# Kernel tuning notes

Measured on AMD Instinct MI355X. Metric: run time of the kernel, lower is better.

## Reference

```python
import jax, jax.numpy as jnp
import numpy as np

DIM = 1024
DIM_HEAD = 64
HEADS = 8
INNER = DIM_HEAD * HEADS
EPS = 1e-5


def layernorm(x, g, b):
    mu = jnp.mean(x, axis=-1, keepdims=True)
    var = jnp.var(x, axis=-1, keepdims=True)
    return (x - mu) * jax.lax.rsqrt(var + EPS) * g + b


def setup_inputs() -> dict:
    key = jax.random.key(0)
    ks = jax.random.split(key, 8)
    b, n, m = 8, 4096, 64
    x = jax.random.normal(ks[0], (b, n, DIM), dtype=jnp.float32)
    latents = jax.random.normal(ks[1], (b, m, DIM), dtype=jnp.float32)
    mask = jax.random.bernoulli(ks[2], 0.9, (b, n))
    s = DIM ** -0.5
    Wq = jax.random.normal(ks[3], (DIM, INNER), dtype=jnp.float32) * s
    Wkv = jax.random.normal(ks[4], (DIM, 2 * INNER), dtype=jnp.float32) * s
    Wo = jax.random.normal(ks[5], (INNER, DIM), dtype=jnp.float32) * (INNER ** -0.5)
    ln_x_g = jnp.ones((DIM,), jnp.float32); ln_x_b = jnp.zeros((DIM,), jnp.float32)
    ln_l_g = jnp.ones((DIM,), jnp.float32); ln_l_b = jnp.zeros((DIM,), jnp.float32)
    ln_o_g = jnp.ones((DIM,), jnp.float32); ln_o_b = jnp.zeros((DIM,), jnp.float32)
    return {"x": x, "latents": latents, "mask": mask,
            "Wq": Wq, "Wkv": Wkv, "Wo": Wo,
            "ln_x_g": ln_x_g, "ln_x_b": ln_x_b,
            "ln_l_g": ln_l_g, "ln_l_b": ln_l_b,
            "ln_o_g": ln_o_g, "ln_o_b": ln_o_b}


def reference(x, latents, mask, Wq, Wkv, Wo, ln_x_g, ln_x_b, ln_l_g, ln_l_b, ln_o_g, ln_o_b):
    scale = DIM_HEAD ** -0.5
    b, m = latents.shape[0], latents.shape[1]
    xn = layernorm(x, ln_x_g, ln_x_b)
    ln = layernorm(latents, ln_l_g, ln_l_b)
    q = ln @ Wq                                   # [b, m, inner]
    kv_in = jnp.concatenate([xn, ln], axis=1)     # [b, n+m, dim]
    kv = kv_in @ Wkv                              # [b, n+m, 2*inner]
    k, v = jnp.split(kv, 2, axis=-1)
    # b n (h d) -> b h n d
    q = q.reshape(b, m, HEADS, DIM_HEAD).transpose(0, 2, 1, 3)
    k = k.reshape(b, k.shape[1], HEADS, DIM_HEAD).transpose(0, 2, 1, 3)
    v = v.reshape(b, v.shape[1], HEADS, DIM_HEAD).transpose(0, 2, 1, 3)
    # NOTE: scale applied twice, faithful to the original module.
    sim = jnp.einsum('bhid,bhjd->bhij', q * scale, k) * scale
    full_mask = jnp.concatenate([mask, jnp.ones((b, m), dtype=bool)], axis=1)  # pad True for latents
    max_neg = -jnp.finfo(sim.dtype).max
    sim = jnp.where(full_mask[:, None, None, :], sim, max_neg)
    attn = jax.nn.softmax(sim.astype(jnp.float32), axis=-1).astype(sim.dtype)
    out = jnp.einsum('bhij,bhjd->bhid', attn, v)
    out = out.transpose(0, 2, 1, 3).reshape(b, m, INNER)
    out = out @ Wo
    return layernorm(out, ln_o_g, ln_o_b)
```

## Files before the change

### kernel.cpp

```cpp
#include <hip/hip_runtime.h>

typedef unsigned short u16;
typedef unsigned int u32;
using f32x4  = __attribute__((ext_vector_type(4))) float;
using short8 = __attribute__((ext_vector_type(8))) short;
using s16x4  = __attribute__((ext_vector_type(4))) short;
using u16x4  = __attribute__((ext_vector_type(4))) unsigned short;

#define DEV __device__ __forceinline__

DEV u16 f2bf(float f) {
  u32 u = __float_as_uint(f);
  u32 r = u + 0x7fffu + ((u >> 16) & 1u);
  return (u16)(r >> 16);
}

DEV void gload_lds16(const void* g, void* l) {
  __builtin_amdgcn_global_load_lds(
      (__attribute__((address_space(1))) void*)g,
      (__attribute__((address_space(3))) void*)l, 16, 0, 0);
}

DEV void block_reduce2(float& a, float& b, float* red) {
#pragma unroll
  for (int m = 1; m < 64; m <<= 1) {
    a += __shfl_xor(a, m);
    b += __shfl_xor(b, m);
  }
  const int wid = threadIdx.x >> 6, lane = threadIdx.x & 63;
  __syncthreads();
  if (lane == 0) { red[wid] = a; red[4 + wid] = b; }
  __syncthreads();
  a = red[0] + red[1] + red[2] + red[3];
  b = red[4] + red[5] + red[6] + red[7];
}

__global__ __launch_bounds__(256) void ln_rows_k(
    const float* __restrict__ X, const float* __restrict__ g,
    const float* __restrict__ be, u16* __restrict__ out, int mode)
{
  __shared__ float red[8];
  const int r = blockIdx.x, t = threadIdx.x;
  const float4 v = *(const float4*)(X + (((size_t)r) << 10) + t * 4);
  float s1 = v.x + v.y + v.z + v.w;
  float s2 = v.x * v.x + v.y * v.y + v.z * v.z + v.w * v.w;
  block_reduce2(s1, s2, red);
  const float mean = s1 * (1.f / 1024.f);
  const float var  = s2 * (1.f / 1024.f) - mean * mean;
  const float rstd = rsqrtf(var + 1e-5f);
  const float4 gv = *(const float4*)(g + t * 4);
  const float4 bv = *(const float4*)(be + t * 4);
  u16x4 o;
  o[0] = f2bf((v.x - mean) * rstd * gv.x + bv.x);
  o[1] = f2bf((v.y - mean) * rstd * gv.y + bv.y);
  o[2] = f2bf((v.z - mean) * rstd * gv.z + bv.z);
  o[3] = f2bf((v.w - mean) * rstd * gv.w + bv.w);
  const size_t orow = (mode == 0)
      ? ((size_t)(r >> 12) * 4160 + (r & 4095))
      : ((size_t)(r >> 6) * 4160 + 4096 + (r & 63));
  *(u16x4*)(out + orow * 1024 + t * 4) = o;
}

__global__ __launch_bounds__(256) void transpose_w_k(
    const float* __restrict__ W, u16* __restrict__ Wt, int K, int N)
{
  __shared__ float tile[32][33];
  const int n0 = blockIdx.x * 32, k0 = blockIdx.y * 32;
  const int tx = threadIdx.x, ty = threadIdx.y;
#pragma unroll
  for (int i = 0; i < 4; ++i)
    tile[ty + 8 * i][tx] = W[(size_t)(k0 + ty + 8 * i) * N + n0 + tx];
  __syncthreads();
#pragma unroll
  for (int i = 0; i < 4; ++i)
    Wt[(size_t)(n0 + ty + 8 * i) * K + k0 + tx] = f2bf(tile[tx][ty + 8 * i]);
}

__global__ __launch_bounds__(256) void mask_bias_k(const void* __restrict__ mask,
                                                   float* __restrict__ bias)
{
  __shared__ int flag_s;
  if (threadIdx.x == 0) {
    const u32* mw = (const u32*)mask;
    bool fpat = true, ipat = true;
    for (int i = 0; i < 256; ++i) {
      u32 w = mw[i];
      if (w != 0u && w != 0x3f800000u) fpat = false;
      if (w > 1u) ipat = false;
    }
    flag_s = fpat ? 2 : (ipat ? 1 : 0);
  }
  __syncthreads();
  const int flag = flag_s;
  const int idx = blockIdx.x * 256 + threadIdx.x;
  const int b = idx / 4160, j = idx - b * 4160;
  float bv = 0.f;
  if (j < 4096) {
    const int mi = b * 4096 + j;
    bool on;
    if (flag == 2)      on = ((const float*)mask)[mi] != 0.f;
    else if (flag == 1) on = ((const int*)mask)[mi] != 0;
    else                on = ((const unsigned char*)mask)[mi] != 0;
    bv = on ? 0.f : -1e30f;
  }
  bias[idx] = bv;
}

__global__ __launch_bounds__(512, 4) void gemm2_k(
    const u16* __restrict__ xnl, const u16* __restrict__ Wq_t,
    const u16* __restrict__ Wkv_t,
    u16* __restrict__ q_h, u16* __restrict__ k_h, u16* __restrict__ v_t)
{
  __shared__ __attribute__((aligned(16))) short As[3][4096];
  __shared__ __attribute__((aligned(16))) short Bs[3][8192];

  const int tid = threadIdx.x, lane = tid & 63;
  const int wid = tid >> 6, wr = wid >> 2, wc = wid & 3;
  const int l15 = lane & 15, lq = lane >> 4;

  const int bid = blockIdx.x;
  int mode, mblk, nblk;
  const u16 *Ap, *Bp;
  if (bid < 1040) {
    const int slab = bid >> 3, s = bid & 7;
    if (s < 4) { mode = 0; mblk = slab * 2 + (s & 1); nblk = s >> 1; Ap = xnl; Bp = Wkv_t; }
    else       { mode = 2; mblk = s - 4; nblk = slab; Ap = Wkv_t + (size_t)512 * 1024; Bp = xnl; }
  } else {
    const int r2 = bid - 1040; mode = 1; mblk = r2 >> 1; nblk = r2 & 1;
    Ap = xnl; Bp = Wq_t;
  }
  const int m0 = mblk * 128, n0 = nblk * 256;

  const int srow = tid >> 2, sslot = tid & 3;
  const u32 ss = (u32)((sslot ^ ((srow >> 1) & 3)) * 8);
  const int gra = m0 + srow;
  const u32 arow = (mode == 1) ? ((u32)(gra >> 6) * 4160u + 4096u + (u32)(gra & 63)) : (u32)gra;
  const u32 aoff  = arow * 1024u + ss;
  const u32 boff0 = (u32)(n0 + srow) * 1024u + ss;
  const u32 boff1 = (u32)(n0 + 128 + srow) * 1024u + ss;

  const int rsw = ((lq ^ ((l15 >> 1) & 3)) << 4);
  const int aRd = wr * 4096 + l15 * 64 + rsw;
  const int bRd = wc * 4096 + l15 * 64 + rsw;

  const f32x4 z4 = {0.f, 0.f, 0.f, 0.f};
  f32x4 acc[4][4];
#pragma unroll
  for (int i = 0; i < 4; ++i)
#pragma unroll
    for (int j = 0; j < 4; ++j) acc[i][j] = z4;

  auto stage = [&](int buf, int T) {
    gload_lds16(Ap + aoff  + (u32)T * 32u, &As[buf][tid * 8]);
    gload_lds16(Bp + boff0 + (u32)T * 32u, &Bs[buf][tid * 8]);
    gload_lds16(Bp + boff1 + (u32)T * 32u, &Bs[buf][4096 + tid * 8]);
  };

  stage(0, 0);
  stage(1, 1);
  asm volatile("s_waitcnt vmcnt(3)" ::: "memory");
  __builtin_amdgcn_s_barrier();

  int c0 = 0, c1 = 1, c2 = 2;
#pragma unroll 1
  for (int t = 0; t < 32; ++t) {
    if (t < 30) stage(c2, t + 2);
    const char* aB = (const char*)&As[0][0] + c0 * 8192  + aRd;
    const char* bB = (const char*)&Bs[0][0] + c0 * 16384 + bRd;
    short8 af[4], bf[4];
#pragma unroll
    for (int mi = 0; mi < 4; ++mi) af[mi] = *(const short8*)(aB + mi * 1024);
#pragma unroll
    for (int nj = 0; nj < 4; ++nj) bf[nj] = *(const short8*)(bB + nj * 1024);
    __builtin_amdgcn_s_setprio(1);
#pragma unroll
    for (int mi = 0; mi < 4; ++mi)
#pragma unroll
      for (int nj = 0; nj < 4; ++nj)
        acc[mi][nj] = __builtin_amdgcn_mfma_f32_16x16x32_bf16(af[mi], bf[nj], acc[mi][nj], 0, 0, 0);
    __builtin_amdgcn_s_setprio(0);
    if (t < 30)       { asm volatile("s_waitcnt vmcnt(3)" ::: "memory"); }
    else if (t == 30) { asm volatile("s_waitcnt vmcnt(0)" ::: "memory"); }
    __builtin_amdgcn_s_barrier();
    const int tmp = c0; c0 = c1; c1 = c2; c2 = tmp;
  }

#pragma unroll
  for (int mi = 0; mi < 4; ++mi)
#pragma unroll
    for (int nj = 0; nj < 4; ++nj)
#pragma unroll
      for (int r = 0; r < 4; ++r) {
        const int gm = m0 + wr * 64 + mi * 16 + lq * 4 + r;
        const int gn = n0 + wc * 64 + nj * 16 + l15;
        const u16 v = f2bf(acc[mi][nj][r]);
        if (mode == 0) {
          const int b = gm / 4160, j = gm - b * 4160;
          k_h[(((size_t)b * 8 + (gn >> 6)) * 4160 + j) * 64 + (gn & 63)] = v;
        } else if (mode == 2) {
          const int b = gn / 4160, j = gn - b * 4160;
          v_t[(((size_t)b * 8 + (gm >> 6)) * 64 + (gm & 63)) * 4160 + j] = v;
        } else {
          const int b = gm >> 6, i2 = gm & 63;
          q_h[(((size_t)b * 8 + (gn >> 6)) * 64 + i2) * 64 + (gn & 63)] = v;
        }
      }
}

__global__ __launch_bounds__(256) void attn_k(
    const u16* __restrict__ q_h, const u16* __restrict__ k_h,
    const u16* __restrict__ v_t, const float* __restrict__ bias,
    float* __restrict__ O_part, float* __restrict__ m_part,
    float* __restrict__ l_part)
{
  __shared__ __attribute__((aligned(16))) short Ks[4096];
  __shared__ __attribute__((aligned(16))) short Vs[4096];
  __shared__ __attribute__((aligned(16))) short Ps[4][1152];
  __shared__ float biasS[64];
  const int bid = blockIdx.x;
  const int sp = bid & 7, bh = bid >> 3;
  const int b = bh >> 3;
  const int tid = threadIdx.x, wid = tid >> 6, lane = tid & 63;
  const int t0 = sp ? (8 * sp + 1) : 0;
  const int tc = sp ? 8 : 9;

  const size_t qoff = ((size_t)bh * 64 + wid * 16 + (lane & 15)) * 64 + 8 * (lane >> 4);
  const short8 qf0 = *(const short8*)&q_h[qoff];
  const short8 qf1 = *(const short8*)&q_h[qoff + 32];

  float mrun = -1e30f, lrun = 0.f;
  const f32x4 z4 = {0.f, 0.f, 0.f, 0.f};
  f32x4 o[4] = {z4, z4, z4, z4};
  const size_t khead = (size_t)bh * (4160 * 64);
  const size_t vhead = (size_t)bh * (64 * 4160);

  for (int tt = 0; tt < tc; ++tt) {
    const int t = t0 + tt;
#pragma unroll
    for (int p = 0; p < 2; ++p) {
      const int lo = (p * 256 + tid) * 16;
      const int row = lo >> 7;
      const int src = lo ^ ((row & 7) << 4);
      gload_lds16((const char*)k_h + (khead + (size_t)t * 4096) * 2 + src,
                  (char*)Ks + (p * 256 + wid * 64) * 16);
    }
#pragma unroll
    for (int p = 0; p < 2; ++p) {
      const int lo = (p * 256 + tid) * 16;
      const int row = lo >> 7;
      const int colb = (lo ^ ((row & 7) << 4)) & 127;
      gload_lds16((const char*)v_t + (vhead + (size_t)row * 4160 + t * 64) * 2 + colb,
                  (char*)Vs + (p * 256 + wid * 64) * 16);
    }
    if (tid < 64) biasS[tid] = bias[b * 4160 + t * 64 + tid];
    __syncthreads();

    f32x4 sc[4] = {z4, z4, z4, z4};
#pragma unroll
    for (int mi = 0; mi < 4; ++mi) {
      const int row = mi * 16 + (lane & 15);
      const int sw = (row & 7) << 4;
      short8 a0 = *(const short8*)((const char*)Ks + ((row * 128 + 16 * (lane >> 4)) ^ sw));
      sc[mi] = __builtin_amdgcn_mfma_f32_16x16x32_bf16(a0, qf0, sc[mi], 0, 0, 0);
      short8 a1 = *(const short8*)((const char*)Ks + ((row * 128 + 64 + 16 * (lane >> 4)) ^ sw));
      sc[mi] = __builtin_amdgcn_mfma_f32_16x16x32_bf16(a1, qf1, sc[mi], 0, 0, 0);
    }

    float sv[4][4];
    float tmax = -3e30f;
#pragma unroll
    for (int mi = 0; mi < 4; ++mi)
#pragma unroll
      for (int r = 0; r < 4; ++r) {
        const int kv = mi * 16 + (lane >> 4) * 4 + r;
        const float s = sc[mi][r] * (1.f / 64.f) + biasS[kv];
        sv[mi][r] = s;
        tmax = fmaxf(tmax, s);
      }
    tmax = fmaxf(tmax, __shfl_xor(tmax, 16));
    tmax = fmaxf(tmax, __shfl_xor(tmax, 32));
    const float mnew = fmaxf(mrun, tmax);
    const float fac = __expf(mrun - mnew);
    float psum = 0.f;
#pragma unroll
    for (int mi = 0; mi < 4; ++mi) {
      s16x4 pk;
#pragma unroll
      for (int r = 0; r < 4; ++r) {
        const float p = __expf(sv[mi][r] - mnew);
        psum += p;
        pk[r] = (short)f2bf(p);
      }
      *(s16x4*)&Ps[wid][(lane & 15) * 72 + mi * 16 + (lane >> 4) * 4] = pk;
    }
    psum += __shfl_xor(psum, 16);
    psum += __shfl_xor(psum, 32);
    lrun = lrun * fac + psum;
    mrun = mnew;
#pragma unroll
    for (int mi = 0; mi < 4; ++mi)
#pragma unroll
      for (int e = 0; e < 4; ++e) o[mi][e] *= fac;

#pragma unroll
    for (int mi = 0; mi < 4; ++mi) {
      const int row = mi * 16 + (lane & 15);
      const int sw = (row & 7) << 4;
      short8 a0 = *(const short8*)((const char*)Vs + ((row * 128 + 16 * (lane >> 4)) ^ sw));
      short8 p0 = *(const short8*)&Ps[wid][(lane & 15) * 72 + 8 * (lane >> 4)];
      o[mi] = __builtin_amdgcn_mfma_f32_16x16x32_bf16(a0, p0, o[mi], 0, 0, 0);
      short8 a1 = *(const short8*)((const char*)Vs + ((row * 128 + 64 + 16 * (lane >> 4)) ^ sw));
      short8 p1 = *(const short8*)&Ps[wid][(lane & 15) * 72 + 32 + 8 * (lane >> 4)];
      o[mi] = __builtin_amdgcn_mfma_f32_16x16x32_bf16(a1, p1, o[mi], 0, 0, 0);
    }
    __syncthreads();
  }

#pragma unroll
  for (int mi = 0; mi < 4; ++mi)
#pragma unroll
    for (int r = 0; r < 4; ++r) {
      const int d = mi * 16 + (lane >> 4) * 4 + r;
      const int q = wid * 16 + (lane & 15);
      O_part[(((size_t)sp * 64 + bh) * 64 + d) * 64 + q] = o[mi][r];
    }
  if (lane < 16) {
    m_part[((size_t)sp * 64 + bh) * 64 + wid * 16 + lane] = mrun;
    l_part[((size_t)sp * 64 + bh) * 64 + wid * 16 + lane] = lrun;
  }
}

__global__ __launch_bounds__(256) void combine_k(
    const float* __restrict__ O_part, const float* __restrict__ m_part,
    const float* __restrict__ l_part, float* __restrict__ attn_out)
{
  __shared__ float wgt[8][64];
  const int bh = blockIdx.x;
  const int b = bh >> 3, h = bh & 7;
  const int t = threadIdx.x;
  if (t < 64) {
    float mv[8], lv[8];
#pragma unroll
    for (int s = 0; s < 8; ++s) {
      mv[s] = m_part[((size_t)s * 64 + bh) * 64 + t];
      lv[s] = l_part[((size_t)s * 64 + bh) * 64 + t];
    }
    float M = mv[0];
#pragma unroll
    for (int s = 1; s < 8; ++s) M = fmaxf(M, mv[s]);
    float den = 0.f;
#pragma unroll
    for (int s = 0; s < 8; ++s) den += lv[s] * __expf(mv[s] - M);
    const float inv = 1.f / den;
#pragma unroll
    for (int s = 0; s < 8; ++s) wgt[s][t] = __expf(mv[s] - M) * inv;
  }
  __syncthreads();
#pragma unroll
  for (int i = 0; i < 16; ++i) {
    const int p = i * 256 + t;
    const int d = p >> 6, q = p & 63;
    float acc = 0.f;
#pragma unroll
    for (int s = 0; s < 8; ++s)
      acc += O_part[(((size_t)s * 64 + bh) * 64 + d) * 64 + q] * wgt[s][q];
    attn_out[((size_t)b * 64 + q) * 512 + h * 64 + d] = acc;
  }
}

__global__ __launch_bounds__(256) void outproj_k(
    const float* __restrict__ attn_out, const float* __restrict__ Wo,
    const float* __restrict__ g, const float* __restrict__ be,
    float* __restrict__ out)
{
  __shared__ float arow[2][512];
  __shared__ float red[8];
  const int rb = blockIdx.x * 2, t = threadIdx.x;
  arow[0][t]       = attn_out[(size_t)rb * 512 + t];
  arow[0][t + 256] = attn_out[(size_t)rb * 512 + 256 + t];
  arow[1][t]       = attn_out[(size_t)(rb + 1) * 512 + t];
  arow[1][t + 256] = attn_out[(size_t)(rb + 1) * 512 + 256 + t];
  __syncthreads();
  float a0x = 0, a0y = 0, a0z = 0, a0w = 0;
  float a1x = 0, a1y = 0, a1z = 0, a1w = 0;
  for (int k = 0; k < 512; ++k) {
    const float4 w = *(const float4*)(Wo + (size_t)k * 1024 + t * 4);
    const float x0 = arow[0][k], x1 = arow[1][k];
    a0x += x0 * w.x; a0y += x0 * w.y; a0z += x0 * w.z; a0w += x0 * w.w;
    a1x += x1 * w.x; a1y += x1 * w.y; a1z += x1 * w.z; a1w += x1 * w.w;
  }
  const float4 gv = *(const float4*)(g + t * 4);
  const float4 bv = *(const float4*)(be + t * 4);
  {
    float s1 = a0x + a0y + a0z + a0w;
    float s2 = a0x * a0x + a0y * a0y + a0z * a0z + a0w * a0w;
    block_reduce2(s1, s2, red);
    const float mean = s1 * (1.f / 1024.f);
    const float rstd = rsqrtf(s2 * (1.f / 1024.f) - mean * mean + 1e-5f);
    float4 ov;
    ov.x = (a0x - mean) * rstd * gv.x + bv.x;
    ov.y = (a0y - mean) * rstd * gv.y + bv.y;
    ov.z = (a0z - mean) * rstd * gv.z + bv.z;
    ov.w = (a0w - mean) * rstd * gv.w + bv.w;
    *(float4*)(out + (size_t)rb * 1024 + t * 4) = ov;
  }
  {
    float s1 = a1x + a1y + a1z + a1w;
    float s2 = a1x * a1x + a1y * a1y + a1z * a1z + a1w * a1w;
    block_reduce2(s1, s2, red);
    const float mean = s1 * (1.f / 1024.f);
    const float rstd = rsqrtf(s2 * (1.f / 1024.f) - mean * mean + 1e-5f);
    float4 ov;
    ov.x = (a1x - mean) * rstd * gv.x + bv.x;
    ov.y = (a1y - mean) * rstd * gv.y + bv.y;
    ov.z = (a1z - mean) * rstd * gv.z + bv.z;
    ov.w = (a1w - mean) * rstd * gv.w + bv.w;
    *(float4*)(out + (size_t)(rb + 1) * 1024 + t * 4) = ov;
  }
}

extern "C" void kernel_launch(void* const* d_in, const int* in_sizes, int n_in,
                              void* d_out, int out_size, void* d_ws, size_t ws_size,
                              hipStream_t stream) {
  (void)in_sizes; (void)n_in; (void)out_size; (void)ws_size;
  const float* x       = (const float*)d_in[0];
  const float* latents = (const float*)d_in[1];
  const void*  mask    = d_in[2];
  const float* Wq      = (const float*)d_in[3];
  const float* Wkv     = (const float*)d_in[4];
  const float* Wo      = (const float*)d_in[5];
  const float* gx      = (const float*)d_in[6];
  const float* bx      = (const float*)d_in[7];
  const float* gl      = (const float*)d_in[8];
  const float* bl      = (const float*)d_in[9];
  const float* go      = (const float*)d_in[10];
  const float* bo      = (const float*)d_in[11];
  float* out = (float*)d_out;

  char* w = (char*)d_ws;
  u16* xnl   = (u16*)w; w += (size_t)33280 * 1024 * 2;
  u16* Wq_t  = (u16*)w; w += (size_t)512 * 1024 * 2;
  u16* Wkv_t = (u16*)w; w += (size_t)1024 * 1024 * 2;
  u16* q_h   = (u16*)w; w += (size_t)8 * 8 * 64 * 64 * 2;
  u16* k_h   = (u16*)w; w += (size_t)8 * 8 * 4160 * 64 * 2;
  u16* v_t   = (u16*)w; w += (size_t)8 * 8 * 64 * 4160 * 2;
  float* bias   = (float*)w; w += (size_t)8 * 4160 * 4;
  float* O_part = (float*)w; w += (size_t)8 * 64 * 64 * 64 * 4;
  float* m_part = (float*)w; w += (size_t)8 * 64 * 64 * 4;
  float* l_part = (float*)w; w += (size_t)8 * 64 * 64 * 4;
  float* attnO  = (float*)w; w += (size_t)512 * 512 * 4;

  transpose_w_k<<<dim3(16, 32), dim3(32, 8), 0, stream>>>(Wq, Wq_t, 1024, 512);
  transpose_w_k<<<dim3(32, 32), dim3(32, 8), 0, stream>>>(Wkv, Wkv_t, 1024, 1024);
  ln_rows_k<<<dim3(32768), dim3(256), 0, stream>>>(x, gx, bx, xnl, 0);
  ln_rows_k<<<dim3(512), dim3(256), 0, stream>>>(latents, gl, bl, xnl, 1);
  mask_bias_k<<<dim3(130), dim3(256), 0, stream>>>(mask, bias);
  gemm2_k<<<dim3(1048), dim3(512), 0, stream>>>(xnl, Wq_t, Wkv_t, q_h, k_h, v_t);
  attn_k<<<dim3(512), dim3(256), 0, stream>>>(q_h, k_h, v_t, bias, O_part, m_part, l_part);
  combine_k<<<dim3(64), dim3(256), 0, stream>>>(O_part, m_part, l_part, attnO);
  outproj_k<<<dim3(256), dim3(256), 0, stream>>>(attnO, Wo, go, bo, out);
}
```

Measured before the change: 246.1 us.

## Load weight fragments directly from global memory into registers in projection GEMM

The fused Q/K/V projection GEMM no longer stages the weight operand through LDS. Each wave reads its weight fragments straight from global memory into registers every k-step, and only the activation tile goes through the triple-buffered LDS pipeline. This halves or more the LDS footprint and LDS read traffic. Block ordering is also regrouped by mode. The cost is exposed global load latency on the weight reads inside the loop, which are not prefetched, plus a lower occupancy hint in launch bounds.

```diff
diff --git a/kernel.cpp b/kernel.cpp
--- a/kernel.cpp
+++ b/kernel.cpp
@@ -106,13 +106,12 @@
   bias[idx] = bv;
 }
 
-__global__ __launch_bounds__(512, 4) void gemm2_k(
+__global__ __launch_bounds__(512, 2) void gemm5_k(
     const u16* __restrict__ xnl, const u16* __restrict__ Wq_t,
     const u16* __restrict__ Wkv_t,
     u16* __restrict__ q_h, u16* __restrict__ k_h, u16* __restrict__ v_t)
 {
-  __shared__ __attribute__((aligned(16))) short As[3][4096];
-  __shared__ __attribute__((aligned(16))) short Bs[3][8192];
+  __shared__ __attribute__((aligned(16))) short Ls[3][8192];
 
   const int tid = threadIdx.x, lane = tid & 63;
   const int wid = tid >> 6, wr = wid >> 2, wc = wid & 3;
@@ -120,28 +119,30 @@
 
   const int bid = blockIdx.x;
   int mode, mblk, nblk;
-  const u16 *Ap, *Bp;
-  if (bid < 1040) {
-    const int slab = bid >> 3, s = bid & 7;
-    if (s < 4) { mode = 0; mblk = slab * 2 + (s & 1); nblk = s >> 1; Ap = xnl; Bp = Wkv_t; }
-    else       { mode = 2; mblk = s - 4; nblk = slab; Ap = Wkv_t + (size_t)512 * 1024; Bp = xnl; }
-  } else {
-    const int r2 = bid - 1040; mode = 1; mblk = r2 >> 1; nblk = r2 & 1;
-    Ap = xnl; Bp = Wq_t;
-  }
+  if (bid < 520)       { mode = 0; mblk = bid >> 1; nblk = bid & 1; }
+  else if (bid < 1040) { const int r2 = bid - 520; mode = 2; mblk = r2 & 3; nblk = r2 >> 2; }
+  else                 { const int r2 = bid - 1040; mode = 1; mblk = r2 >> 1; nblk = r2 & 1; }
   const int m0 = mblk * 128, n0 = nblk * 256;
 
   const int srow = tid >> 2, sslot = tid & 3;
   const u32 ss = (u32)((sslot ^ ((srow >> 1) & 3)) * 8);
-  const int gra = m0 + srow;
-  const u32 arow = (mode == 1) ? ((u32)(gra >> 6) * 4160u + 4096u + (u32)(gra & 63)) : (u32)gra;
-  const u32 aoff  = arow * 1024u + ss;
-  const u32 boff0 = (u32)(n0 + srow) * 1024u + ss;
-  const u32 boff1 = (u32)(n0 + 128 + srow) * 1024u + ss;
-
-  const int rsw = ((lq ^ ((l15 >> 1) & 3)) << 4);
-  const int aRd = wr * 4096 + l15 * 64 + rsw;
-  const int bRd = wc * 4096 + l15 * 64 + rsw;
+  u32 lsrc0 = 0, lsrc1 = 0;
+  if (mode == 2) {
+    lsrc0 = (u32)(n0 + srow) * 1024u + ss;
+    lsrc1 = (u32)(n0 + 128 + srow) * 1024u + ss;
+  } else {
+    const int gr = m0 + srow;
+    const u32 ar = (mode == 1) ? ((u32)(gr >> 6) * 4160u + 4096u + (u32)(gr & 63)) : (u32)gr;
+    lsrc0 = ar * 1024u + ss;
+  }
+
+  const int rslot = lq ^ ((l15 >> 1) & 3);
+  const int lRd = ((mode == 2 ? wc : wr) * 64 + l15) * 32 + rslot * 8;
+
+  const u16* Wb = (mode == 0) ? Wkv_t
+                : (mode == 1 ? Wq_t : Wkv_t + (size_t)512 * 1024);
+  const int wRowBase = (mode == 2) ? (m0 + wr * 64 + l15) : (n0 + wc * 64 + l15);
+  const u32 wOff = (u32)wRowBase * 1024u + (u32)(lq * 8);
 
   const f32x4 z4 = {0.f, 0.f, 0.f, 0.f};
   f32x4 acc[4][4];
@@ -151,36 +152,49 @@
     for (int j = 0; j < 4; ++j) acc[i][j] = z4;
 
   auto stage = [&](int buf, int T) {
-    gload_lds16(Ap + aoff  + (u32)T * 32u, &As[buf][tid * 8]);
-    gload_lds16(Bp + boff0 + (u32)T * 32u, &Bs[buf][tid * 8]);
-    gload_lds16(Bp + boff1 + (u32)T * 32u, &Bs[buf][4096 + tid * 8]);
+    gload_lds16(xnl + lsrc0 + (u32)T * 32u, &Ls[buf][tid * 8]);
+    if (mode == 2) gload_lds16(xnl + lsrc1 + (u32)T * 32u, &Ls[buf][4096 + tid * 8]);
   };
 
   stage(0, 0);
   stage(1, 1);
-  asm volatile("s_waitcnt vmcnt(3)" ::: "memory");
+  if (mode == 2) { asm volatile("s_waitcnt vmcnt(2)" ::: "memory"); }
+  else           { asm volatile("s_waitcnt vmcnt(1)" ::: "memory"); }
   __builtin_amdgcn_s_barrier();
 
   int c0 = 0, c1 = 1, c2 = 2;
 #pragma unroll 1
   for (int t = 0; t < 32; ++t) {
+    short8 wf[4];
+#pragma unroll
+    for (int j = 0; j < 4; ++j)
+      wf[j] = *(const short8*)(Wb + wOff + (u32)(j * 16384) + (u32)(t * 32));
     if (t < 30) stage(c2, t + 2);
-    const char* aB = (const char*)&As[0][0] + c0 * 8192  + aRd;
-    const char* bB = (const char*)&Bs[0][0] + c0 * 16384 + bRd;
-    short8 af[4], bf[4];
-#pragma unroll
-    for (int mi = 0; mi < 4; ++mi) af[mi] = *(const short8*)(aB + mi * 1024);
-#pragma unroll
-    for (int nj = 0; nj < 4; ++nj) bf[nj] = *(const short8*)(bB + nj * 1024);
+    const short* lB = &Ls[0][0] + c0 * 8192 + lRd;
+    short8 lf[4];
+#pragma unroll
+    for (int i = 0; i < 4; ++i) lf[i] = *(const short8*)(lB + i * 512);
     __builtin_amdgcn_s_setprio(1);
-#pragma unroll
-    for (int mi = 0; mi < 4; ++mi)
-#pragma unroll
-      for (int nj = 0; nj < 4; ++nj)
-        acc[mi][nj] = __builtin_amdgcn_mfma_f32_16x16x32_bf16(af[mi], bf[nj], acc[mi][nj], 0, 0, 0);
+    if (mode == 2) {
+#pragma unroll
+      for (int mi = 0; mi < 4; ++mi)
+#pragma unroll
+        for (int nj = 0; nj < 4; ++nj)
+          acc[mi][nj] = __builtin_amdgcn_mfma_f32_16x16x32_bf16(wf[mi], lf[nj], acc[mi][nj], 0, 0, 0);
+    } else {
+#pragma unroll
+      for (int mi = 0; mi < 4; ++mi)
+#pragma unroll
+        for (int nj = 0; nj < 4; ++nj)
+          acc[mi][nj] = __builtin_amdgcn_mfma_f32_16x16x32_bf16(lf[mi], wf[nj], acc[mi][nj], 0, 0, 0);
+    }
     __builtin_amdgcn_s_setprio(0);
-    if (t < 30)       { asm volatile("s_waitcnt vmcnt(3)" ::: "memory"); }
-    else if (t == 30) { asm volatile("s_waitcnt vmcnt(0)" ::: "memory"); }
+    if (t < 30) {
+      if (mode == 2) { asm volatile("s_waitcnt vmcnt(2)" ::: "memory"); }
+      else           { asm volatile("s_waitcnt vmcnt(1)" ::: "memory"); }
+    } else if (t == 30) {
+      asm volatile("s_waitcnt vmcnt(0)" ::: "memory");
+    }
     __builtin_amdgcn_s_barrier();
     const int tmp = c0; c0 = c1; c1 = c2; c2 = tmp;
   }
@@ -455,7 +469,7 @@
   ln_rows_k<<<dim3(32768), dim3(256), 0, stream>>>(x, gx, bx, xnl, 0);
   ln_rows_k<<<dim3(512), dim3(256), 0, stream>>>(latents, gl, bl, xnl, 1);
   mask_bias_k<<<dim3(130), dim3(256), 0, stream>>>(mask, bias);
-  gemm2_k<<<dim3(1048), dim3(512), 0, stream>>>(xnl, Wq_t, Wkv_t, q_h, k_h, v_t);
+  gemm5_k<<<dim3(1048), dim3(512), 0, stream>>>(xnl, Wq_t, Wkv_t, q_h, k_h, v_t);
   attn_k<<<dim3(512), dim3(256), 0, stream>>>(q_h, k_h, v_t, bias, O_part, m_part, l_part);
   combine_k<<<dim3(64), dim3(256), 0, stream>>>(O_part, m_part, l_part, attnO);
   outproj_k<<<dim3(256), dim3(256), 0, stream>>>(attnO, Wo, go, bo, out);
```

New measurement: 403.4 us. 63.9% more time.
